# Optimization experiments

Measured on AMD Instinct MI355X. Metric: run time of the kernel, lower is better.

Reference implementation:

```python
import jax, jax.numpy as jnp
import numpy as np

F, V, D, B = 3, 512, 8192, 64


def setup_inputs() -> dict:
    key = jax.random.key(0)
    k1, k2 = jax.random.split(key)
    # bipolar (MAP) codebooks: (f, v, d) in {-1, +1}
    codebooks = jnp.sign(jax.random.normal(k1, (F, V, D), dtype=jnp.float32))
    codebooks = jnp.where(codebooks == 0, 1.0, codebooks)
    # ground-truth factors -> inputs = bind (elementwise product) of one codevector per factor
    idx = jax.random.randint(k2, (B, F), 0, V)
    picked = codebooks[jnp.arange(F)[None, :], idx]          # (b, f, d)
    inputs = jnp.prod(picked, axis=1)                         # (b, d)
    # init estimates: bundle (superposition) of each codebook, signed, broadcast to batch
    init = jnp.sign(jnp.sum(codebooks, axis=1))               # (f, d)
    init = jnp.where(init == 0, 1.0, init)
    init_estimates = jnp.broadcast_to(init, (B, F, D)).astype(jnp.float32)
    return {"inputs": inputs, "init_estimates": init_estimates,
            "codebooks": codebooks, "iterations": 10}


def reference(inputs, init_estimates, codebooks, iterations):
    f = init_estimates.shape[-2]

    def step(est):
        # MAP inverse is identity; inv_others[:, j] = prod_{i != j} est[:, i]
        rolled = jnp.stack([jnp.roll(est, i, axis=-2) for i in range(1, f)], axis=-2)  # (b,f,f-1,d)
        inv_others = jnp.prod(rolled, axis=-2)                 # (b, f, d)  multibind
        new_est = inputs[:, None, :] * inv_others              # bind       (b, f, d)
        sim = jnp.einsum('bfd,fvd->bfv', new_est, codebooks)   # codebook similarity
        return jnp.sign(jnp.einsum('bfv,fvd->bfd', sim, codebooks))

    def cond(c):
        est, old, cnt, done = c
        return (cnt < iterations) & jnp.logical_not(done)

    def body(c):
        est, old, cnt, done = c
        new = step(est)
        done = jnp.all(new == old)
        return (new, new, cnt + 1, done)

    carry0 = (init_estimates, init_estimates, jnp.int32(0), jnp.array(False))
    est, _, cnt, _ = jax.lax.while_loop(cond, body, carry0)

    # cleanup: nearest codevector per factor (argmax dot similarity)
    sims = jnp.einsum('bfd,fvd->bfv', est, codebooks)
    outcome = jnp.argmax(sims, axis=-1)                        # (b, f) int indices
    return outcome, cnt - 1
```

## Files before the change

### kernel.cpp

```cpp
#include <hip/hip_runtime.h>

#define F 3
#define V 512
#define D 8192
#define B 64
#define ITERS 10

typedef __bf16 bf16_t;
typedef __bf16 bf16x8 __attribute__((ext_vector_type(8)));
typedef __bf16 bf16x4 __attribute__((ext_vector_type(4)));
typedef float f32x4 __attribute__((ext_vector_type(4)));

__global__ void k_init_ew(const float* __restrict__ cod, const float* __restrict__ ie,
                          bf16_t* __restrict__ Cb, bf16_t* __restrict__ est0,
                          float* __restrict__ simBase, int* __restrict__ anydiff) {
  long tid = (long)blockIdx.x * blockDim.x + threadIdx.x;
  long NT  = (long)gridDim.x * blockDim.x;
  for (long i = tid * 4; i < (long)F * V * D; i += NT * 4) {
    f32x4 x = *(const f32x4*)(cod + i);
    bf16x4 y;
    y[0] = (bf16_t)x[0]; y[1] = (bf16_t)x[1]; y[2] = (bf16_t)x[2]; y[3] = (bf16_t)x[3];
    *(bf16x4*)(Cb + i) = y;
  }
  for (long i = tid * 4; i < (long)B * F * D; i += NT * 4) {
    f32x4 x = *(const f32x4*)(ie + i);
    bf16x4 y;
    y[0] = (bf16_t)x[0]; y[1] = (bf16_t)x[1]; y[2] = (bf16_t)x[2]; y[3] = (bf16_t)x[3];
    *(bf16x4*)(est0 + i) = y;
  }
  f32x4 z = {0.f, 0.f, 0.f, 0.f};
  for (long i = tid * 4; i < (long)(ITERS + 1) * F * B * V; i += NT * 4)
    *(f32x4*)(simBase + i) = z;
  if (tid < 16) anydiff[tid] = 0;
}

__global__ __launch_bounds__(256) void k_init_tr(const float* __restrict__ Csrc,
                                                 bf16_t* __restrict__ CbT) {
  int f = blockIdx.z, vt = blockIdx.y, dt = blockIdx.x;
  __shared__ bf16_t tile[64 * 65];
  int t = threadIdx.x;
  int v0 = vt * 64, d0 = dt * 64;
#pragma unroll
  for (int p = 0; p < 16; ++p) {
    int q = t + 256 * p;
    int i = q >> 6, j = q & 63;
    tile[i * 65 + j] = (bf16_t)Csrc[((long)(f * V + v0 + i)) * D + d0 + j];
  }
  __syncthreads();
#pragma unroll
  for (int p = 0; p < 16; ++p) {
    int q = t + 256 * p;
    int jj = q >> 6, ii = q & 63;
    CbT[((long)f * D + d0 + jj) * V + v0 + ii] = tile[ii * 65 + jj];
  }
}

__global__ __launch_bounds__(256) void k_sim(const float* __restrict__ inputs,
                                             const bf16_t* __restrict__ Cb,
                                             const bf16_t* __restrict__ est0,
                                             const bf16_t* __restrict__ est1,
                                             float* __restrict__ simBase,
                                             const int* __restrict__ anydiff, int iter) {
  const int f = blockIdx.z, vt = blockIdx.y, ks = blockIdx.x;
  const bf16_t* est;
  float* sim;
  const bool is_final = (iter >= ITERS);
  if (is_final) {
    int first0 = ITERS;
    for (int i = 0; i < ITERS; ++i) {
      if (anydiff[i] == 0) { first0 = i; break; }
    }
    int par = (first0 < ITERS) ? ((first0 + 1) & 1) : 0;
    est = par ? est1 : est0;
    sim = simBase + (long)ITERS * (F * B * V);
  } else {
    for (int i = 0; i < iter; ++i)
      if (anydiff[i] == 0) return;
    est = (iter & 1) ? est1 : est0;
    sim = simBase + (long)iter * (F * B * V);
  }
  const int f1 = (f + 1) % 3, f2 = (f + 2) % 3;

  __shared__ __attribute__((aligned(16))) bf16_t lA[64 * 88];
  __shared__ __attribute__((aligned(16))) bf16_t lB[64 * 88];

  const int t = threadIdx.x;
  const int lane = t & 63, w = t >> 6;
  const int lm = lane & 15, quad = lane >> 4;

  f32x4 zero = {0.f, 0.f, 0.f, 0.f};
  f32x4 acc[4];
#pragma unroll
  for (int mt = 0; mt < 4; ++mt) acc[mt] = zero;

  const int v0 = vt * 64;
  const int dbase = ks * 1024;

  for (int c = 0; c < 16; ++c) {
    const int d0 = dbase + c * 64;
    __syncthreads();
#pragma unroll
    for (int p = 0; p < 2; ++p) {
      int q = t + 256 * p;
      int b = q >> 3, dd = (q & 7) * 8;
      if (is_final) {
        *(bf16x8*)&lA[b * 88 + dd] =
            *(const bf16x8*)(est + ((long)b * F + f) * D + d0 + dd);
      } else {
        const float* ip = inputs + (long)b * D + d0 + dd;
        bf16x8 e1 = *(const bf16x8*)(est + ((long)b * F + f1) * D + d0 + dd);
        bf16x8 e2 = *(const bf16x8*)(est + ((long)b * F + f2) * D + d0 + dd);
        bf16x8 o;
#pragma unroll
        for (int i = 0; i < 8; ++i)
          o[i] = (bf16_t)(ip[i] * (float)e1[i] * (float)e2[i]);
        *(bf16x8*)&lA[b * 88 + dd] = o;
      }
    }
#pragma unroll
    for (int p = 0; p < 2; ++p) {
      int q = t + 256 * p;
      int v = q >> 3, dd = (q & 7) * 8;
      *(bf16x8*)&lB[v * 88 + dd] =
          *(const bf16x8*)(Cb + ((long)(f * V + v0 + v)) * D + d0 + dd);
    }
    __syncthreads();
#pragma unroll
    for (int ks2 = 0; ks2 < 2; ++ks2) {
      const int kb = ks2 * 32 + quad * 8;
      bf16x8 bfrag = *(const bf16x8*)&lB[(w * 16 + lm) * 88 + kb];
#pragma unroll
      for (int mt = 0; mt < 4; ++mt) {
        bf16x8 afrag = *(const bf16x8*)&lA[(mt * 16 + lm) * 88 + kb];
        acc[mt] = __builtin_amdgcn_mfma_f32_16x16x32_bf16(afrag, bfrag, acc[mt], 0, 0, 0);
      }
    }
  }
  const int v = v0 + w * 16 + lm;
#pragma unroll
  for (int mt = 0; mt < 4; ++mt)
#pragma unroll
    for (int r = 0; r < 4; ++r) {
      int b = mt * 16 + quad * 4 + r;
      atomicAdd(&sim[(f * B + b) * V + v], acc[mt][r]);
    }
}

__global__ __launch_bounds__(256) void k_upd(const float* __restrict__ simBase,
                                             const bf16_t* __restrict__ CbT,
                                             bf16_t* __restrict__ est0,
                                             bf16_t* __restrict__ est1,
                                             int* __restrict__ anydiff, int iter) {
  const int f = blockIdx.y;
  const int d0 = blockIdx.x * 128;
  for (int i = 0; i < iter; ++i)
    if (anydiff[i] == 0) return;
  const bf16_t* estIn = (iter & 1) ? est1 : est0;
  bf16_t* estOut = (iter & 1) ? est0 : est1;
  const float* sim = simBase + (long)iter * (F * B * V) + f * (B * V);

  __shared__ __attribute__((aligned(16))) bf16_t lAh[64 * 88];
  __shared__ __attribute__((aligned(16))) bf16_t lAl[64 * 88];
  __shared__ __attribute__((aligned(16))) bf16_t lB[128 * 88];

  const int t = threadIdx.x;
  const int lane = t & 63, w = t >> 6;
  const int lm = lane & 15, quad = lane >> 4;

  f32x4 zero = {0.f, 0.f, 0.f, 0.f};
  f32x4 accH[4][2], accL[4][2];
#pragma unroll
  for (int mt = 0; mt < 4; ++mt)
#pragma unroll
    for (int nt = 0; nt < 2; ++nt) { accH[mt][nt] = zero; accL[mt][nt] = zero; }

  for (int c = 0; c < 8; ++c) {
    const int vb = c * 64;
    __syncthreads();
#pragma unroll
    for (int p = 0; p < 2; ++p) {
      int q = t + 256 * p;
      int b = q >> 3, vv = (q & 7) * 8;
      const float* sp = sim + b * V + vb + vv;
#pragma unroll
      for (int i = 0; i < 8; ++i) {
        int si = (int)sp[i];
        lAh[b * 88 + vv + i] = (bf16_t)(float)(si >> 8);
        lAl[b * 88 + vv + i] = (bf16_t)(float)(si & 255);
      }
    }
#pragma unroll
    for (int p = 0; p < 4; ++p) {
      int q = t + 256 * p;
      int r = q >> 3, vv = (q & 7) * 8;
      *(bf16x8*)&lB[r * 88 + vv] =
          *(const bf16x8*)(CbT + ((long)f * D + d0 + r) * V + vb + vv);
    }
    __syncthreads();
#pragma unroll
    for (int ks2 = 0; ks2 < 2; ++ks2) {
      const int kb = ks2 * 32 + quad * 8;
      bf16x8 bf0 = *(const bf16x8*)&lB[(w * 32 + lm) * 88 + kb];
      bf16x8 bf1 = *(const bf16x8*)&lB[(w * 32 + 16 + lm) * 88 + kb];
#pragma unroll
      for (int mt = 0; mt < 4; ++mt) {
        bf16x8 ah = *(const bf16x8*)&lAh[(mt * 16 + lm) * 88 + kb];
        bf16x8 al = *(const bf16x8*)&lAl[(mt * 16 + lm) * 88 + kb];
        accH[mt][0] = __builtin_amdgcn_mfma_f32_16x16x32_bf16(ah, bf0, accH[mt][0], 0, 0, 0);
        accH[mt][1] = __builtin_amdgcn_mfma_f32_16x16x32_bf16(ah, bf1, accH[mt][1], 0, 0, 0);
        accL[mt][0] = __builtin_amdgcn_mfma_f32_16x16x32_bf16(al, bf0, accL[mt][0], 0, 0, 0);
        accL[mt][1] = __builtin_amdgcn_mfma_f32_16x16x32_bf16(al, bf1, accL[mt][1], 0, 0, 0);
      }
    }
  }
  bool anyd = false;
#pragma unroll
  for (int mt = 0; mt < 4; ++mt)
#pragma unroll
    for (int nt = 0; nt < 2; ++nt)
#pragma unroll
      for (int r = 0; r < 4; ++r) {
        int b = mt * 16 + quad * 4 + r;
        int d = d0 + w * 32 + nt * 16 + lm;
        float val = 256.f * accH[mt][nt][r] + accL[mt][nt][r];
        float s = (val > 0.f) ? 1.f : ((val < 0.f) ? -1.f : 0.f);
        long idx = ((long)b * F + f) * D + d;
        estOut[idx] = (bf16_t)s;
        anyd |= ((float)estIn[idx] != s);
      }
  if (__any(anyd) && lane == 0) atomicOr(&anydiff[iter], 1);
}

__global__ __launch_bounds__(64) void k_out(const float* __restrict__ simBase,
                                            const int* __restrict__ anydiff,
                                            int* __restrict__ out) {
  const float* sim = simBase + (long)ITERS * (F * B * V);
  int bid = blockIdx.x;
  int b = bid / F, f = bid % F;
  int lane = threadIdx.x;
  const float* row = sim + (f * B + b) * V;
  float best = -1e30f;
  int bidx = 0;
#pragma unroll
  for (int i = 0; i < V / 64; ++i) {
    int v = lane + 64 * i;
    float x = row[v];
    if (x > best) { best = x; bidx = v; }
  }
  for (int off = 32; off; off >>= 1) {
    float ov = __shfl_down(best, off, 64);
    int oi = __shfl_down(bidx, off, 64);
    if (ov > best || (ov == best && oi < bidx)) { best = ov; bidx = oi; }
  }
  if (lane == 0) out[b * F + f] = bidx;
  if (bid == 0 && lane == 0) {
    int first0 = ITERS;
    for (int i = 0; i < ITERS; ++i) {
      if (anydiff[i] == 0) { first0 = i; break; }
    }
    int cnt = (first0 < ITERS) ? (first0 + 1) : ITERS;
    out[B * F] = cnt - 1;
  }
}

extern "C" void kernel_launch(void* const* d_in, const int* in_sizes, int n_in,
                              void* d_out, int out_size, void* d_ws, size_t ws_size,
                              hipStream_t stream) {
  const float* inputs    = (const float*)d_in[0];
  const float* init_est  = (const float*)d_in[1];
  const float* codebooks = (const float*)d_in[2];

  char* w = (char*)d_ws;
  size_t o = 0;
  auto alloc = [&](size_t bytes) -> void* {
    void* p = w + o;
    o = (o + bytes + 255) & ~(size_t)255;
    return p;
  };
  bf16_t* Cb   = (bf16_t*)alloc((size_t)F * V * D * 2);
  bf16_t* CbT  = (bf16_t*)alloc((size_t)F * D * V * 2);
  bf16_t* est0 = (bf16_t*)alloc((size_t)B * F * D * 2);
  bf16_t* est1 = (bf16_t*)alloc((size_t)B * F * D * 2);
  float* simBase = (float*)alloc((size_t)(ITERS + 1) * F * B * V * 4);
  int* anydiff = (int*)alloc(64);

  k_init_ew<<<2048, 256, 0, stream>>>(codebooks, init_est, Cb, est0, simBase, anydiff);
  k_init_tr<<<dim3(128, 8, 3), 256, 0, stream>>>(codebooks, CbT);

  for (int j = 0; j < ITERS; ++j) {
    k_sim<<<dim3(8, 8, 3), 256, 0, stream>>>(inputs, Cb, est0, est1, simBase, anydiff, j);
    k_upd<<<dim3(64, 3), 256, 0, stream>>>(simBase, CbT, est0, est1, anydiff, j);
  }
  k_sim<<<dim3(8, 8, 3), 256, 0, stream>>>(inputs, Cb, est0, est1, simBase, anydiff, ITERS);
  k_out<<<B * F, 64, 0, stream>>>(simBase, anydiff, (int*)d_out);
}
```

Baseline: 611.5 us.

## Load codebook MFMA fragments directly from global and double grid parallelism

The sim and update kernels now read codebook B-fragments straight from global memory into registers instead of staging them through shared memory. Each K chunk grows to 128, the sim split-K goes from 8 to 16 and the update tile narrows from 128 to 64 columns, so each launch gets twice as many blocks. Codebook conversion is also fused into the transpose kernel, which saves one full read of the fp32 codebook. The cost is uncoalesced 16-byte global loads per lane with no LDS reuse, and twice as many atomic adds in sim.

```diff
diff --git a/kernel.cpp b/kernel.cpp
--- a/kernel.cpp
+++ b/kernel.cpp
@@ -11,17 +11,10 @@
 typedef __bf16 bf16x4 __attribute__((ext_vector_type(4)));
 typedef float f32x4 __attribute__((ext_vector_type(4)));
 
-__global__ void k_init_ew(const float* __restrict__ cod, const float* __restrict__ ie,
-                          bf16_t* __restrict__ Cb, bf16_t* __restrict__ est0,
-                          float* __restrict__ simBase, int* __restrict__ anydiff) {
+__global__ void k_init_small(const float* __restrict__ ie, bf16_t* __restrict__ est0,
+                             float* __restrict__ simBase, int* __restrict__ anydiff) {
   long tid = (long)blockIdx.x * blockDim.x + threadIdx.x;
   long NT  = (long)gridDim.x * blockDim.x;
-  for (long i = tid * 4; i < (long)F * V * D; i += NT * 4) {
-    f32x4 x = *(const f32x4*)(cod + i);
-    bf16x4 y;
-    y[0] = (bf16_t)x[0]; y[1] = (bf16_t)x[1]; y[2] = (bf16_t)x[2]; y[3] = (bf16_t)x[3];
-    *(bf16x4*)(Cb + i) = y;
-  }
   for (long i = tid * 4; i < (long)B * F * D; i += NT * 4) {
     f32x4 x = *(const f32x4*)(ie + i);
     bf16x4 y;
@@ -34,7 +27,8 @@
   if (tid < 16) anydiff[tid] = 0;
 }
 
-__global__ __launch_bounds__(256) void k_init_tr(const float* __restrict__ Csrc,
+__global__ __launch_bounds__(256) void k_init_cb(const float* __restrict__ Csrc,
+                                                 bf16_t* __restrict__ Cb,
                                                  bf16_t* __restrict__ CbT) {
   int f = blockIdx.z, vt = blockIdx.y, dt = blockIdx.x;
   __shared__ bf16_t tile[64 * 65];
@@ -44,7 +38,9 @@
   for (int p = 0; p < 16; ++p) {
     int q = t + 256 * p;
     int i = q >> 6, j = q & 63;
-    tile[i * 65 + j] = (bf16_t)Csrc[((long)(f * V + v0 + i)) * D + d0 + j];
+    bf16_t x = (bf16_t)Csrc[((long)(f * V + v0 + i)) * D + d0 + j];
+    tile[i * 65 + j] = x;
+    Cb[((long)(f * V + v0 + i)) * D + d0 + j] = x;
   }
   __syncthreads();
 #pragma unroll
@@ -67,9 +63,8 @@
   const bool is_final = (iter >= ITERS);
   if (is_final) {
     int first0 = ITERS;
-    for (int i = 0; i < ITERS; ++i) {
+    for (int i = 0; i < ITERS; ++i)
       if (anydiff[i] == 0) { first0 = i; break; }
-    }
     int par = (first0 < ITERS) ? ((first0 + 1) & 1) : 0;
     est = par ? est1 : est0;
     sim = simBase + (long)ITERS * (F * B * V);
@@ -81,8 +76,7 @@
   }
   const int f1 = (f + 1) % 3, f2 = (f + 2) % 3;
 
-  __shared__ __attribute__((aligned(16))) bf16_t lA[64 * 88];
-  __shared__ __attribute__((aligned(16))) bf16_t lB[64 * 88];
+  __shared__ __attribute__((aligned(16))) bf16_t lA[64 * 136];
 
   const int t = threadIdx.x;
   const int lane = t & 63, w = t >> 6;
@@ -94,44 +88,42 @@
   for (int mt = 0; mt < 4; ++mt) acc[mt] = zero;
 
   const int v0 = vt * 64;
-  const int dbase = ks * 1024;
-
-  for (int c = 0; c < 16; ++c) {
-    const int d0 = dbase + c * 64;
-    __syncthreads();
-#pragma unroll
-    for (int p = 0; p < 2; ++p) {
+  const int dbase = ks * 512;
+  const bf16_t* bp = Cb + ((long)(f * V + v0 + w * 16 + lm)) * D + dbase;
+
+  for (int c = 0; c < 4; ++c) {
+    const int d0c = dbase + c * 128;
+    __syncthreads();
+#pragma unroll
+    for (int p = 0; p < 4; ++p) {
       int q = t + 256 * p;
-      int b = q >> 3, dd = (q & 7) * 8;
+      int b = q >> 4, dd = (q & 15) * 8;
       if (is_final) {
-        *(bf16x8*)&lA[b * 88 + dd] =
-            *(const bf16x8*)(est + ((long)b * F + f) * D + d0 + dd);
+        *(bf16x8*)&lA[b * 136 + dd] =
+            *(const bf16x8*)(est + ((long)b * F + f) * D + d0c + dd);
       } else {
-        const float* ip = inputs + (long)b * D + d0 + dd;
-        bf16x8 e1 = *(const bf16x8*)(est + ((long)b * F + f1) * D + d0 + dd);
-        bf16x8 e2 = *(const bf16x8*)(est + ((long)b * F + f2) * D + d0 + dd);
+        const float* ip = inputs + (long)b * D + d0c + dd;
+        f32x4 x0 = *(const f32x4*)ip;
+        f32x4 x1 = *(const f32x4*)(ip + 4);
+        bf16x8 e1 = *(const bf16x8*)(est + ((long)b * F + f1) * D + d0c + dd);
+        bf16x8 e2 = *(const bf16x8*)(est + ((long)b * F + f2) * D + d0c + dd);
         bf16x8 o;
 #pragma unroll
-        for (int i = 0; i < 8; ++i)
-          o[i] = (bf16_t)(ip[i] * (float)e1[i] * (float)e2[i]);
-        *(bf16x8*)&lA[b * 88 + dd] = o;
-      }
-    }
-#pragma unroll
-    for (int p = 0; p < 2; ++p) {
-      int q = t + 256 * p;
-      int v = q >> 3, dd = (q & 7) * 8;
-      *(bf16x8*)&lB[v * 88 + dd] =
-          *(const bf16x8*)(Cb + ((long)(f * V + v0 + v)) * D + d0 + dd);
-    }
-    __syncthreads();
-#pragma unroll
-    for (int ks2 = 0; ks2 < 2; ++ks2) {
+        for (int i = 0; i < 4; ++i) {
+          o[i]     = (bf16_t)(x0[i] * (float)e1[i]     * (float)e2[i]);
+          o[i + 4] = (bf16_t)(x1[i] * (float)e1[i + 4] * (float)e2[i + 4]);
+        }
+        *(bf16x8*)&lA[b * 136 + dd] = o;
+      }
+    }
+    __syncthreads();
+#pragma unroll
+    for (int ks2 = 0; ks2 < 4; ++ks2) {
       const int kb = ks2 * 32 + quad * 8;
-      bf16x8 bfrag = *(const bf16x8*)&lB[(w * 16 + lm) * 88 + kb];
+      bf16x8 bfrag = *(const bf16x8*)(bp + c * 128 + kb);
 #pragma unroll
       for (int mt = 0; mt < 4; ++mt) {
-        bf16x8 afrag = *(const bf16x8*)&lA[(mt * 16 + lm) * 88 + kb];
+        bf16x8 afrag = *(const bf16x8*)&lA[(mt * 16 + lm) * 136 + kb];
         acc[mt] = __builtin_amdgcn_mfma_f32_16x16x32_bf16(afrag, bfrag, acc[mt], 0, 0, 0);
       }
     }
@@ -152,82 +144,72 @@
                                              bf16_t* __restrict__ est1,
                                              int* __restrict__ anydiff, int iter) {
   const int f = blockIdx.y;
-  const int d0 = blockIdx.x * 128;
+  const int d0 = blockIdx.x * 64;
   for (int i = 0; i < iter; ++i)
     if (anydiff[i] == 0) return;
   const bf16_t* estIn = (iter & 1) ? est1 : est0;
   bf16_t* estOut = (iter & 1) ? est0 : est1;
   const float* sim = simBase + (long)iter * (F * B * V) + f * (B * V);
 
-  __shared__ __attribute__((aligned(16))) bf16_t lAh[64 * 88];
-  __shared__ __attribute__((aligned(16))) bf16_t lAl[64 * 88];
-  __shared__ __attribute__((aligned(16))) bf16_t lB[128 * 88];
+  __shared__ __attribute__((aligned(16))) bf16_t lAh[64 * 136];
+  __shared__ __attribute__((aligned(16))) bf16_t lAl[64 * 136];
 
   const int t = threadIdx.x;
   const int lane = t & 63, w = t >> 6;
   const int lm = lane & 15, quad = lane >> 4;
 
   f32x4 zero = {0.f, 0.f, 0.f, 0.f};
-  f32x4 accH[4][2], accL[4][2];
-#pragma unroll
-  for (int mt = 0; mt < 4; ++mt)
-#pragma unroll
-    for (int nt = 0; nt < 2; ++nt) { accH[mt][nt] = zero; accL[mt][nt] = zero; }
-
-  for (int c = 0; c < 8; ++c) {
-    const int vb = c * 64;
-    __syncthreads();
-#pragma unroll
-    for (int p = 0; p < 2; ++p) {
+  f32x4 accH[4], accL[4];
+#pragma unroll
+  for (int mt = 0; mt < 4; ++mt) { accH[mt] = zero; accL[mt] = zero; }
+
+  const bf16_t* bp = CbT + ((long)f * D + d0 + w * 16 + lm) * V;
+
+  for (int c = 0; c < 4; ++c) {
+    const int vb = c * 128;
+    __syncthreads();
+#pragma unroll
+    for (int p = 0; p < 4; ++p) {
       int q = t + 256 * p;
-      int b = q >> 3, vv = (q & 7) * 8;
+      int b = q >> 4, vv = (q & 15) * 8;
       const float* sp = sim + b * V + vb + vv;
+      bf16x8 h, l;
 #pragma unroll
       for (int i = 0; i < 8; ++i) {
         int si = (int)sp[i];
-        lAh[b * 88 + vv + i] = (bf16_t)(float)(si >> 8);
-        lAl[b * 88 + vv + i] = (bf16_t)(float)(si & 255);
-      }
-    }
-#pragma unroll
-    for (int p = 0; p < 4; ++p) {
-      int q = t + 256 * p;
-      int r = q >> 3, vv = (q & 7) * 8;
-      *(bf16x8*)&lB[r * 88 + vv] =
-          *(const bf16x8*)(CbT + ((long)f * D + d0 + r) * V + vb + vv);
-    }
-    __syncthreads();
-#pragma unroll
-    for (int ks2 = 0; ks2 < 2; ++ks2) {
+        h[i] = (bf16_t)(float)(si >> 8);
+        l[i] = (bf16_t)(float)(si & 255);
+      }
+      *(bf16x8*)&lAh[b * 136 + vv] = h;
+      *(bf16x8*)&lAl[b * 136 + vv] = l;
+    }
+    __syncthreads();
+#pragma unroll
+    for (int ks2 = 0; ks2 < 4; ++ks2) {
       const int kb = ks2 * 32 + quad * 8;
-      bf16x8 bf0 = *(const bf16x8*)&lB[(w * 32 + lm) * 88 + kb];
-      bf16x8 bf1 = *(const bf16x8*)&lB[(w * 32 + 16 + lm) * 88 + kb];
+      bf16x8 bfrag = *(const bf16x8*)(bp + vb + kb);
 #pragma unroll
       for (int mt = 0; mt < 4; ++mt) {
-        bf16x8 ah = *(const bf16x8*)&lAh[(mt * 16 + lm) * 88 + kb];
-        bf16x8 al = *(const bf16x8*)&lAl[(mt * 16 + lm) * 88 + kb];
-        accH[mt][0] = __builtin_amdgcn_mfma_f32_16x16x32_bf16(ah, bf0, accH[mt][0], 0, 0, 0);
-        accH[mt][1] = __builtin_amdgcn_mfma_f32_16x16x32_bf16(ah, bf1, accH[mt][1], 0, 0, 0);
-        accL[mt][0] = __builtin_amdgcn_mfma_f32_16x16x32_bf16(al, bf0, accL[mt][0], 0, 0, 0);
-        accL[mt][1] = __builtin_amdgcn_mfma_f32_16x16x32_bf16(al, bf1, accL[mt][1], 0, 0, 0);
+        bf16x8 ah = *(const bf16x8*)&lAh[(mt * 16 + lm) * 136 + kb];
+        bf16x8 al = *(const bf16x8*)&lAl[(mt * 16 + lm) * 136 + kb];
+        accH[mt] = __builtin_amdgcn_mfma_f32_16x16x32_bf16(ah, bfrag, accH[mt], 0, 0, 0);
+        accL[mt] = __builtin_amdgcn_mfma_f32_16x16x32_bf16(al, bfrag, accL[mt], 0, 0, 0);
       }
     }
   }
   bool anyd = false;
+  const int d = d0 + w * 16 + lm;
 #pragma unroll
   for (int mt = 0; mt < 4; ++mt)
 #pragma unroll
-    for (int nt = 0; nt < 2; ++nt)
-#pragma unroll
-      for (int r = 0; r < 4; ++r) {
-        int b = mt * 16 + quad * 4 + r;
-        int d = d0 + w * 32 + nt * 16 + lm;
-        float val = 256.f * accH[mt][nt][r] + accL[mt][nt][r];
-        float s = (val > 0.f) ? 1.f : ((val < 0.f) ? -1.f : 0.f);
-        long idx = ((long)b * F + f) * D + d;
-        estOut[idx] = (bf16_t)s;
-        anyd |= ((float)estIn[idx] != s);
-      }
+    for (int r = 0; r < 4; ++r) {
+      int b = mt * 16 + quad * 4 + r;
+      float val = 256.f * accH[mt][r] + accL[mt][r];
+      float s = (val > 0.f) ? 1.f : ((val < 0.f) ? -1.f : 0.f);
+      long idx = ((long)b * F + f) * D + d;
+      estOut[idx] = (bf16_t)s;
+      anyd |= ((float)estIn[idx] != s);
+    }
   if (__any(anyd) && lane == 0) atomicOr(&anydiff[iter], 1);
 }
 
@@ -255,9 +237,8 @@
   if (lane == 0) out[b * F + f] = bidx;
   if (bid == 0 && lane == 0) {
     int first0 = ITERS;
-    for (int i = 0; i < ITERS; ++i) {
+    for (int i = 0; i < ITERS; ++i)
       if (anydiff[i] == 0) { first0 = i; break; }
-    }
     int cnt = (first0 < ITERS) ? (first0 + 1) : ITERS;
     out[B * F] = cnt - 1;
   }
@@ -284,13 +265,13 @@
   float* simBase = (float*)alloc((size_t)(ITERS + 1) * F * B * V * 4);
   int* anydiff = (int*)alloc(64);
 
-  k_init_ew<<<2048, 256, 0, stream>>>(codebooks, init_est, Cb, est0, simBase, anydiff);
-  k_init_tr<<<dim3(128, 8, 3), 256, 0, stream>>>(codebooks, CbT);
+  k_init_small<<<1024, 256, 0, stream>>>(init_est, est0, simBase, anydiff);
+  k_init_cb<<<dim3(128, 8, 3), 256, 0, stream>>>(codebooks, Cb, CbT);
 
   for (int j = 0; j < ITERS; ++j) {
-    k_sim<<<dim3(8, 8, 3), 256, 0, stream>>>(inputs, Cb, est0, est1, simBase, anydiff, j);
-    k_upd<<<dim3(64, 3), 256, 0, stream>>>(simBase, CbT, est0, est1, anydiff, j);
-  }
-  k_sim<<<dim3(8, 8, 3), 256, 0, stream>>>(inputs, Cb, est0, est1, simBase, anydiff, ITERS);
+    k_sim<<<dim3(16, 8, 3), 256, 0, stream>>>(inputs, Cb, est0, est1, simBase, anydiff, j);
+    k_upd<<<dim3(128, 3), 256, 0, stream>>>(simBase, CbT, est0, est1, anydiff, j);
+  }
+  k_sim<<<dim3(16, 8, 3), 256, 0, stream>>>(inputs, Cb, est0, est1, simBase, anydiff, ITERS);
   k_out<<<B * F, 64, 0, stream>>>(simBase, anydiff, (int*)d_out);
 }
```

After: 621.0 us. No clear change (+1.6%).
